# Optimization experiments

Hardware: AMD Instinct MI355X
Metric: run time of the kernel (lower is better)

Reference implementation:

```python
import jax, jax.numpy as jnp
import numpy as np

N_NODES = 50000
N_EDGES = 800000
D_IN = 128
D_OUT = 1


def setup_inputs() -> dict:
    key = jax.random.key(0)
    k1, k2, k3, k4 = jax.random.split(key, 4)
    X = jax.random.normal(k1, (N_NODES, D_IN), dtype=jnp.float32)
    edge_index = jax.random.randint(k2, (2, N_EDGES), 0, N_NODES, dtype=jnp.int64)
    # SAGEConv params: lin_l (with bias) applied to max-aggregated neighbors,
    # lin_r (no bias) applied to root/self features.
    scale = 1.0 / np.sqrt(D_IN)
    W_l = jax.random.uniform(k3, (D_OUT, D_IN), jnp.float32, -scale, scale)
    b_l = jnp.zeros((D_OUT,), jnp.float32)
    W_r = jax.random.uniform(k4, (D_OUT, D_IN), jnp.float32, -scale, scale)
    return {"X": X, "W_l": W_l, "b_l": b_l, "W_r": W_r, "edge_index": edge_index}


def reference(X, W_l, b_l, W_r, edge_index):
    # SAGEConv(aggr='max', root_weight=True, normalize=False):
    #   out_i = W_l @ max_{j in N(i)} x_j + b_l + W_r @ x_i
    src = edge_index[0]  # message sources (x_j)
    dst = edge_index[1]  # aggregation targets
    # scatter-max of gathered neighbor features; empty segments -> 0 (PyG fill)
    agg = jax.ops.segment_max(X[src], dst, num_segments=X.shape[0])  # [N, D_IN]
    agg = jnp.where(jnp.isfinite(agg), agg, jnp.zeros_like(agg))
    return agg @ W_l.T + b_l + X @ W_r.T  # [N, D_OUT]
```

## Files before the change

kernel.cpp:

```cpp
#include <hip/hip_runtime.h>

#define N_NODES 50000
#define N_EDGES 800000
#define D_IN    128
#define CAP     64

#define NBKT    196
#define BCAP    4864
#define EPT     16
#define EPB     (256 * EPT)
#define SPLIT_BLOCKS ((N_EDGES + EPB - 1) / EPB)
#define CVT_BLOCKS   ((N_NODES * 64 + 255) / 256)


__device__ __forceinline__ unsigned short f32_to_bf16_rn(float f) {
    unsigned int u = __float_as_uint(f);
    u += 0x7fffu + ((u >> 16) & 1u);
    return (unsigned short)(u >> 16);
}

__global__ __launch_bounds__(256) void k_zero(int* __restrict__ gctr)
{
    if (threadIdx.x < NBKT) gctr[threadIdx.x] = 0;
}

__global__ __launch_bounds__(256) void k_split_cvt(
    const int*   __restrict__ src,
    const int*   __restrict__ dst,
    int*         __restrict__ gctr,
    unsigned int* __restrict__ staging,
    const float* __restrict__ X,
    const float* __restrict__ W_r,
    const float* __restrict__ b_l,
    unsigned short* __restrict__ Xh,
    float*       __restrict__ selfdot)
{
    int b = blockIdx.x;
    if (b < SPLIT_BLOCKS) {
        __shared__ int hist[NBKT];
        __shared__ int base[NBKT];
        int tid = threadIdx.x;
        for (int i = tid; i < NBKT; i += 256) hist[i] = 0;
        __syncthreads();

        int t[EPT], s[EPT], bk[EPT];
        bool ok[EPT];
        int e0 = b * EPB + tid;
#pragma unroll
        for (int k = 0; k < EPT; ++k) {
            int e = e0 + (k << 8);
            bool v = e < N_EDGES;
            int ec = v ? e : 0;
            t[k] = dst[ec]; s[k] = src[ec];
            bk[k] = t[k] >> 8;
            ok[k] = v;
            if (v) atomicAdd(&hist[bk[k]], 1);
        }
        __syncthreads();
        for (int i = tid; i < NBKT; i += 256) {
            int h = hist[i];
            base[i] = h ? atomicAdd(&gctr[i], h) : 0;
            hist[i] = 0;
        }
        __syncthreads();
#pragma unroll
        for (int k = 0; k < EPT; ++k) {
            if (ok[k]) {
                int pos = base[bk[k]] + atomicAdd(&hist[bk[k]], 1);
                if (pos < BCAP)
                    staging[bk[k] * BCAP + pos] =
                        ((unsigned int)(t[k] & 255) << 16) | (unsigned int)s[k];
            }
        }
        return;
    }
    int wave = ((b - SPLIT_BLOCKS) * 256 + threadIdx.x) >> 6;
    int lane = threadIdx.x & 63;
    if (wave >= N_NODES) return;

    float2 x = ((const float2*)(X + (size_t)wave * D_IN))[lane];
    unsigned int packed = ((unsigned int)f32_to_bf16_rn(x.y) << 16)
                        |  (unsigned int)f32_to_bf16_rn(x.x);
    ((unsigned int*)(Xh + (size_t)wave * D_IN))[lane] = packed;

    float2 wr = ((const float2*)W_r)[lane];
    float acc = x.x * wr.x + x.y * wr.y;
#pragma unroll
    for (int off = 32; off; off >>= 1)
        acc += __shfl_down(acc, off);
    if (lane == 0)
        selfdot[wave] = acc + b_l[0];
}

__global__ __launch_bounds__(256) void k_build(
    const unsigned int* __restrict__ staging,
    const int*   __restrict__ gctr,
    int*         __restrict__ cnt,
    unsigned short* __restrict__ sorted16)
{
    __shared__ unsigned short lbuf[256 * CAP];
    __shared__ int lcnt[256];
    int b   = blockIdx.x;
    int tid = threadIdx.x;
    lcnt[tid] = 0;
    __syncthreads();

    int count = gctr[b];
    if (count > BCAP) count = BCAP;
    for (int i = tid; i < count; i += 256) {
        unsigned int rec = staging[b * BCAP + i];
        int nlo = rec >> 16;
        int pos = atomicAdd(&lcnt[nlo], 1);
        if (pos < CAP)
            lbuf[nlo * CAP + pos] = (unsigned short)(rec & 0xffffu);
    }
    __syncthreads();

    int nodebase = b << 8;
    int node = nodebase + tid;
    if (node < N_NODES) {
        int c = lcnt[tid];
        cnt[node] = c < CAP ? c : CAP;
    }
    int nrows = N_NODES - nodebase;
    if (nrows > 256) nrows = 256;
    int tot32 = nrows * (CAP / 2);
    const unsigned int* lb32 = (const unsigned int*)lbuf;
    unsigned int* out32 = (unsigned int*)(sorted16 + (size_t)nodebase * CAP);
    for (int i = tid; i < tot32; i += 256)
        out32[i] = lb32[i];
}

#define GATHER(mm, ss)                                                \
    {                                                                 \
        unsigned int u = Xu[(size_t)(ss) * 64 + lane];                \
        (mm).x = fmaxf((mm).x, __uint_as_float(u << 16));             \
        (mm).y = fmaxf((mm).y, __uint_as_float(u & 0xffff0000u));     \
    }

__global__ __launch_bounds__(256) void k_agg(
    const unsigned short* __restrict__ Xh,
    const int*   __restrict__ cnt,
    const unsigned short* __restrict__ sorted16,
    const float* __restrict__ W_l,
    const float* __restrict__ selfdot,
    float*       __restrict__ out)
{
    int wave = (blockIdx.x * 256 + threadIdx.x) >> 6;
    int lane = threadIdx.x & 63;
    if (wave >= N_NODES) return;

    int n = cnt[wave];
    int sid = (int)sorted16[wave * CAP + lane];
    if (n > CAP) n = CAP;

    float2 wl = ((const float2*)W_l)[lane];
    float sd  = selfdot[wave];

    const unsigned int* Xu = (const unsigned int*)Xh;
    float2 m[8];
#pragma unroll
    for (int k = 0; k < 8; ++k) m[k] = make_float2(-INFINITY, -INFINITY);

    int i = 0;
    for (; i + 8 <= n; i += 8) {
        int s0 = __shfl(sid, i + 0), s1 = __shfl(sid, i + 1);
        int s2 = __shfl(sid, i + 2), s3 = __shfl(sid, i + 3);
        int s4 = __shfl(sid, i + 4), s5 = __shfl(sid, i + 5);
        int s6 = __shfl(sid, i + 6), s7 = __shfl(sid, i + 7);
        GATHER(m[0], s0) GATHER(m[1], s1) GATHER(m[2], s2) GATHER(m[3], s3)
        GATHER(m[4], s4) GATHER(m[5], s5) GATHER(m[6], s6) GATHER(m[7], s7)
    }
    if (i + 4 <= n) {
        int s0 = __shfl(sid, i + 0), s1 = __shfl(sid, i + 1);
        int s2 = __shfl(sid, i + 2), s3 = __shfl(sid, i + 3);
        GATHER(m[0], s0) GATHER(m[1], s1) GATHER(m[2], s2) GATHER(m[3], s3)
        i += 4;
    }
    if (i + 2 <= n) {
        int s0 = __shfl(sid, i + 0), s1 = __shfl(sid, i + 1);
        GATHER(m[0], s0) GATHER(m[1], s1)
        i += 2;
    }
    if (i < n) {
        int s0 = __shfl(sid, i);
        GATHER(m[0], s0)
    }
#pragma unroll
    for (int k = 4; k; k >>= 1)
#pragma unroll
        for (int j = 0; j < k; ++j) {
            m[j].x = fmaxf(m[j].x, m[j + k].x);
            m[j].y = fmaxf(m[j].y, m[j + k].y);
        }
    if (n == 0) { m[0].x = 0.0f; m[0].y = 0.0f; }

    float acc = m[0].x * wl.x + m[0].y * wl.y;
#pragma unroll
    for (int off = 32; off; off >>= 1)
        acc += __shfl_down(acc, off);
    if (lane == 0)
        out[wave] = acc + sd;
}

extern "C" void kernel_launch(void* const* d_in, const int* in_sizes, int n_in,
                              void* d_out, int out_size, void* d_ws, size_t ws_size,
                              hipStream_t stream)
{
    const float* X   = (const float*)d_in[0];
    const float* W_l = (const float*)d_in[1];
    const float* b_l = (const float*)d_in[2];
    const float* W_r = (const float*)d_in[3];
    const int*   ei  = (const int*)d_in[4];
    const int*   src = ei;
    const int*   dst = ei + N_EDGES;

    int* gctr = (int*)d_ws;
    unsigned int* staging = (unsigned int*)(gctr + 256);
    int* cnt = (int*)(staging + (size_t)NBKT * BCAP);
    unsigned short* sorted16 = (unsigned short*)(cnt + N_NODES);
    unsigned short* Xh = sorted16 + (size_t)N_NODES * CAP;
    float* selfdot = (float*)(Xh + (size_t)N_NODES * D_IN);
    float* out = (float*)d_out;

    k_zero<<<1, 256, 0, stream>>>(gctr);
    k_split_cvt<<<SPLIT_BLOCKS + CVT_BLOCKS, 256, 0, stream>>>(
        src, dst, gctr, staging, X, W_r, b_l, Xh, selfdot);
    k_build<<<NBKT, 256, 0, stream>>>(staging, gctr, cnt, sorted16);
    k_agg<<<(N_NODES * 64 + 255) / 256, 256, 0, stream>>>(
        Xh, cnt, sorted16, W_l, selfdot, out);
}
```

Baseline: 67.40 us.

## Fuse bucket build and max-aggregation into one kernel with 64-node buckets

Shrinks buckets from 256 to 64 nodes (782 buckets) and merges the per-bucket local sort with the gather/max aggregation in a single kernel. Neighbor lists now stay in shared memory instead of being written out as sorted16/cnt and read back, and one kernel launch is removed. Each wave processes 16 nodes serially, reading indices from LDS rather than via shuffles. With 782 blocks of 256 threads, each wave works through a longer serial chain, which may cost parallelism and latency hiding in the gather. Buckets holding more than 1280 edges would drop edges.

New measurement: 69.26 us. 2.8% more time.

```diff
diff --git a/kernel.cpp b/kernel.cpp
--- a/kernel.cpp
+++ b/kernel.cpp
@@ -5,8 +5,8 @@
 #define D_IN    128
 #define CAP     64
 
-#define NBKT    196
-#define BCAP    4864
+#define NBKT    782
+#define BCAP    1280
 #define EPT     16
 #define EPB     (256 * EPT)
 #define SPLIT_BLOCKS ((N_EDGES + EPB - 1) / EPB)
@@ -21,7 +21,8 @@
 
 __global__ __launch_bounds__(256) void k_zero(int* __restrict__ gctr)
 {
-    if (threadIdx.x < NBKT) gctr[threadIdx.x] = 0;
+    int i = blockIdx.x * 256 + threadIdx.x;
+    if (i < NBKT) gctr[i] = 0;
 }
 
 __global__ __launch_bounds__(256) void k_split_cvt(
@@ -52,7 +53,7 @@
             bool v = e < N_EDGES;
             int ec = v ? e : 0;
             t[k] = dst[ec]; s[k] = src[ec];
-            bk[k] = t[k] >> 8;
+            bk[k] = t[k] >> 6;
             ok[k] = v;
             if (v) atomicAdd(&hist[bk[k]], 1);
         }
@@ -68,8 +69,8 @@
             if (ok[k]) {
                 int pos = base[bk[k]] + atomicAdd(&hist[bk[k]], 1);
                 if (pos < BCAP)
-                    staging[bk[k] * BCAP + pos] =
-                        ((unsigned int)(t[k] & 255) << 16) | (unsigned int)s[k];
+                    staging[(size_t)bk[k] * BCAP + pos] =
+                        ((unsigned int)(t[k] & 63) << 16) | (unsigned int)s[k];
             }
         }
         return;
@@ -90,45 +91,6 @@
         acc += __shfl_down(acc, off);
     if (lane == 0)
         selfdot[wave] = acc + b_l[0];
-}
-
-__global__ __launch_bounds__(256) void k_build(
-    const unsigned int* __restrict__ staging,
-    const int*   __restrict__ gctr,
-    int*         __restrict__ cnt,
-    unsigned short* __restrict__ sorted16)
-{
-    __shared__ unsigned short lbuf[256 * CAP];
-    __shared__ int lcnt[256];
-    int b   = blockIdx.x;
-    int tid = threadIdx.x;
-    lcnt[tid] = 0;
-    __syncthreads();
-
-    int count = gctr[b];
-    if (count > BCAP) count = BCAP;
-    for (int i = tid; i < count; i += 256) {
-        unsigned int rec = staging[b * BCAP + i];
-        int nlo = rec >> 16;
-        int pos = atomicAdd(&lcnt[nlo], 1);
-        if (pos < CAP)
-            lbuf[nlo * CAP + pos] = (unsigned short)(rec & 0xffffu);
-    }
-    __syncthreads();
-
-    int nodebase = b << 8;
-    int node = nodebase + tid;
-    if (node < N_NODES) {
-        int c = lcnt[tid];
-        cnt[node] = c < CAP ? c : CAP;
-    }
-    int nrows = N_NODES - nodebase;
-    if (nrows > 256) nrows = 256;
-    int tot32 = nrows * (CAP / 2);
-    const unsigned int* lb32 = (const unsigned int*)lbuf;
-    unsigned int* out32 = (unsigned int*)(sorted16 + (size_t)nodebase * CAP);
-    for (int i = tid; i < tot32; i += 256)
-        out32[i] = lb32[i];
 }
 
 #define GATHER(mm, ss)                                                \
@@ -137,70 +99,81 @@
         (mm).x = fmaxf((mm).x, __uint_as_float(u << 16));             \
         (mm).y = fmaxf((mm).y, __uint_as_float(u & 0xffff0000u));     \
     }
-
-__global__ __launch_bounds__(256) void k_agg(
+#define GB(K, I)                                                      \
+    {                                                                 \
+        int sr[K];                                                    \
+        _Pragma("unroll")                                             \
+        for (int k = 0; k < K; ++k) sr[k] = seg[(I) + k];             \
+        _Pragma("unroll")                                             \
+        for (int k = 0; k < K; ++k) GATHER(m[k], sr[k])               \
+    }
+
+__global__ __launch_bounds__(256) void k_bagg(
+    const unsigned int* __restrict__ staging,
+    const int*   __restrict__ gctr,
     const unsigned short* __restrict__ Xh,
-    const int*   __restrict__ cnt,
-    const unsigned short* __restrict__ sorted16,
     const float* __restrict__ W_l,
     const float* __restrict__ selfdot,
     float*       __restrict__ out)
 {
-    int wave = (blockIdx.x * 256 + threadIdx.x) >> 6;
-    int lane = threadIdx.x & 63;
-    if (wave >= N_NODES) return;
-
-    int n = cnt[wave];
-    int sid = (int)sorted16[wave * CAP + lane];
-    if (n > CAP) n = CAP;
-
+    __shared__ unsigned short lbuf[64 * CAP];
+    __shared__ int lcnt[64];
+    int b   = blockIdx.x;
+    int tid = threadIdx.x;
+    if (tid < 64) lcnt[tid] = 0;
+    __syncthreads();
+
+    int count = gctr[b];
+    if (count > BCAP) count = BCAP;
+    for (int i = tid; i < count; i += 256) {
+        unsigned int rec = staging[(size_t)b * BCAP + i];
+        int nlo = rec >> 16;
+        int pos = atomicAdd(&lcnt[nlo], 1);
+        if (pos < CAP)
+            lbuf[nlo * CAP + pos] = (unsigned short)(rec & 0xffffu);
+    }
+    __syncthreads();
+
+    int wid  = tid >> 6;
+    int lane = tid & 63;
     float2 wl = ((const float2*)W_l)[lane];
-    float sd  = selfdot[wave];
-
     const unsigned int* Xu = (const unsigned int*)Xh;
-    float2 m[8];
-#pragma unroll
-    for (int k = 0; k < 8; ++k) m[k] = make_float2(-INFINITY, -INFINITY);
-
-    int i = 0;
-    for (; i + 8 <= n; i += 8) {
-        int s0 = __shfl(sid, i + 0), s1 = __shfl(sid, i + 1);
-        int s2 = __shfl(sid, i + 2), s3 = __shfl(sid, i + 3);
-        int s4 = __shfl(sid, i + 4), s5 = __shfl(sid, i + 5);
-        int s6 = __shfl(sid, i + 6), s7 = __shfl(sid, i + 7);
-        GATHER(m[0], s0) GATHER(m[1], s1) GATHER(m[2], s2) GATHER(m[3], s3)
-        GATHER(m[4], s4) GATHER(m[5], s5) GATHER(m[6], s6) GATHER(m[7], s7)
-    }
-    if (i + 4 <= n) {
-        int s0 = __shfl(sid, i + 0), s1 = __shfl(sid, i + 1);
-        int s2 = __shfl(sid, i + 2), s3 = __shfl(sid, i + 3);
-        GATHER(m[0], s0) GATHER(m[1], s1) GATHER(m[2], s2) GATHER(m[3], s3)
-        i += 4;
-    }
-    if (i + 2 <= n) {
-        int s0 = __shfl(sid, i + 0), s1 = __shfl(sid, i + 1);
-        GATHER(m[0], s0) GATHER(m[1], s1)
-        i += 2;
-    }
-    if (i < n) {
-        int s0 = __shfl(sid, i);
-        GATHER(m[0], s0)
-    }
-#pragma unroll
-    for (int k = 4; k; k >>= 1)
-#pragma unroll
-        for (int j = 0; j < k; ++j) {
-            m[j].x = fmaxf(m[j].x, m[j + k].x);
-            m[j].y = fmaxf(m[j].y, m[j + k].y);
-        }
-    if (n == 0) { m[0].x = 0.0f; m[0].y = 0.0f; }
-
-    float acc = m[0].x * wl.x + m[0].y * wl.y;
-#pragma unroll
-    for (int off = 32; off; off >>= 1)
-        acc += __shfl_down(acc, off);
-    if (lane == 0)
-        out[wave] = acc + sd;
+
+    for (int j = 0; j < 16; ++j) {
+        int li   = (wid << 4) + j;
+        int node = (b << 6) + li;
+        if (node >= N_NODES) return;
+        float sd = selfdot[node];
+        int n = lcnt[li];
+        if (n > CAP) n = CAP;
+        const unsigned short* seg = &lbuf[li * CAP];
+
+        float2 m[8];
+#pragma unroll
+        for (int k = 0; k < 8; ++k) m[k] = make_float2(-INFINITY, -INFINITY);
+
+        int i = 0;
+        for (; i + 8 <= n; i += 8) GB(8, i)
+        if (i + 4 <= n) { GB(4, i) i += 4; }
+        if (i + 2 <= n) { GB(2, i) i += 2; }
+        if (i < n)      { GB(1, i) }
+
+#pragma unroll
+        for (int k = 4; k; k >>= 1)
+#pragma unroll
+            for (int q = 0; q < k; ++q) {
+                m[q].x = fmaxf(m[q].x, m[q + k].x);
+                m[q].y = fmaxf(m[q].y, m[q + k].y);
+            }
+        if (n == 0) { m[0].x = 0.0f; m[0].y = 0.0f; }
+
+        float acc = m[0].x * wl.x + m[0].y * wl.y;
+#pragma unroll
+        for (int off = 32; off; off >>= 1)
+            acc += __shfl_down(acc, off);
+        if (lane == 0)
+            out[node] = acc + sd;
+    }
 }
 
 extern "C" void kernel_launch(void* const* d_in, const int* in_sizes, int n_in,
@@ -216,17 +189,13 @@
     const int*   dst = ei + N_EDGES;
 
     int* gctr = (int*)d_ws;
-    unsigned int* staging = (unsigned int*)(gctr + 256);
-    int* cnt = (int*)(staging + (size_t)NBKT * BCAP);
-    unsigned short* sorted16 = (unsigned short*)(cnt + N_NODES);
-    unsigned short* Xh = sorted16 + (size_t)N_NODES * CAP;
+    unsigned int* staging = (unsigned int*)(gctr + 1024);
+    unsigned short* Xh = (unsigned short*)(staging + (size_t)NBKT * BCAP);
     float* selfdot = (float*)(Xh + (size_t)N_NODES * D_IN);
     float* out = (float*)d_out;
 
-    k_zero<<<1, 256, 0, stream>>>(gctr);
+    k_zero<<<(NBKT + 255) / 256, 256, 0, stream>>>(gctr);
     k_split_cvt<<<SPLIT_BLOCKS + CVT_BLOCKS, 256, 0, stream>>>(
         src, dst, gctr, staging, X, W_r, b_l, Xh, selfdot);
-    k_build<<<NBKT, 256, 0, stream>>>(staging, gctr, cnt, sorted16);
-    k_agg<<<(N_NODES * 64 + 255) / 256, 256, 0, stream>>>(
-        Xh, cnt, sorted16, W_l, selfdot, out);
-}
+    k_bagg<<<NBKT, 256, 0, stream>>>(staging, gctr, Xh, W_l, selfdot, out);
+}
```
